# Performance work log

Measured on AMD Instinct MI355X. Metric: run time of the kernel, lower is better.

The kernel has to match this reference:

```python
import jax, jax.numpy as jnp
import numpy as np

V = 100000   # num_regular_embeddings (full vocab)
K = 20000    # num custom (Poincare) embeddings
P = 300      # custom embedding dim
E = 256      # regular / output embedding dim
B = 1024
L = 256


def logmap0(v):
    # project from Poincare ball (c=1) to tangent space at origin
    norm = jnp.linalg.norm(v, axis=-1, keepdims=True)
    safe = jnp.where(norm > 0, norm, 0.5)            # avoid 0/0 and arctanh(0)/0
    scale = jnp.where(norm > 0, jnp.arctanh(safe) / safe, 1.0)
    return scale * v


def mobius_add(x, y):
    x2 = jnp.sum(x * x, axis=-1, keepdims=True)
    y2 = jnp.sum(y * y, axis=-1, keepdims=True)
    xy = jnp.sum(x * y, axis=-1, keepdims=True)
    num = (1 + 2 * xy + y2) * x + (1 - x2) * y
    denom = jnp.maximum(1 + 2 * xy + x2 * y2, 1e-15)
    return num / denom


def setup_inputs() -> dict:
    key = jax.random.key(0)
    k_x, k_perm, k_cw, k_rw, k_lw = jax.random.split(key, 5)

    x = jax.random.randint(k_x, (B, L), 0, V, dtype=jnp.int32)

    # K distinct custom vocab indices, excluding 0 (padding)
    custom_indices = jax.random.permutation(k_perm, jnp.arange(1, V, dtype=jnp.int32))[:K]

    # vocab -> custom table index (1..K), 0 for non-custom
    vocab_to_custom = jnp.zeros((V,), dtype=jnp.int32).at[custom_indices].set(
        jnp.arange(1, K + 1, dtype=jnp.int32))
    # vocab -> regular table index (0..V-K-1) for non-custom slots
    regular_vocab = jnp.where(vocab_to_custom == 0)[0]  # concrete, size V-K
    vocab_to_regular = jnp.zeros((V,), dtype=jnp.int32).at[regular_vocab].set(
        jnp.arange(V - K, dtype=jnp.int32))

    # fixed (pretrained, frozen) custom weights inside unit ball; row 0 = padding
    custom_fixed_w = (jax.random.normal(k_cw, (K + 1, P), dtype=jnp.float32) * 0.02).at[0].set(0.0)
    # trainable custom table initialized to zeros (as in the module)
    custom_train_w = jnp.zeros((K + 1, P), dtype=jnp.float32)
    # regular embedding table, row 0 = padding
    regular_w = (jax.random.normal(k_rw, (V - K, E), dtype=jnp.float32) * 0.02).at[0].set(0.0)
    # linear transform P -> E
    lin_w = jax.random.normal(k_lw, (E, P), dtype=jnp.float32) * 0.05
    lin_b = jnp.zeros((E,), dtype=jnp.float32)

    return {"x": x, "custom_indices": custom_indices,
            "vocab_to_custom": vocab_to_custom, "vocab_to_regular": vocab_to_regular,
            "custom_fixed_w": custom_fixed_w, "custom_train_w": custom_train_w,
            "regular_w": regular_w, "lin_w": lin_w, "lin_b": lin_b}


def reference(x, custom_indices, vocab_to_custom, vocab_to_regular,
              custom_fixed_w, custom_train_w, regular_w, lin_w, lin_b):
    mask = jnp.isin(x, custom_indices)                     # [B, L]
    custom_feat = jnp.where(mask, x, 0)
    regular_feat = jnp.where(mask, 0, x)

    cm = vocab_to_custom[custom_feat]                      # [B, L]
    fixed = logmap0(custom_fixed_w[cm])                    # [B, L, P]
    train = custom_train_w[cm]                             # [B, L, P]
    custom_emb = mobius_add(fixed, train)                  # [B, L, P]

    regular_emb = regular_w[vocab_to_regular[regular_feat]]  # [B, L, E]

    custom_emb = jnp.einsum("blp,ep->ble", custom_emb, lin_w) + lin_b
    return custom_emb + regular_emb
```

## Files before the change

### kernel.cpp

```cpp
#include <hip/hip_runtime.h>
#include <stdint.h>
#include <math.h>

#define NTOK (1024 * 256)
#define CPY_TOK 256
#define CUS_TOK 128
#define P_DIM 300
#define P_PAD 320
#define P_LDS 328
#define E_DIM 256

typedef __attribute__((ext_vector_type(8))) short bf16x8_t;
typedef __attribute__((ext_vector_type(4))) float f32x4_t;

__device__ __forceinline__ unsigned short f2b(float f) {
    union { float f; unsigned int i; } v; v.f = f;
    unsigned int x = v.i;
    return (unsigned short)((x + 0x7FFFu + ((x >> 16) & 1u)) >> 16);
}

__global__ __launch_bounds__(256) void kA_copy(
        const int* __restrict__ x, const int* __restrict__ v2r,
        const float* __restrict__ regular_w, const float* __restrict__ lin_b,
        const float* __restrict__ lin_w, unsigned short* __restrict__ lin_w_pad,
        float* __restrict__ out) {
    int tid  = threadIdx.x;
    int wid  = tid >> 6;
    int lane = tid & 63;

    if (blockIdx.x < (E_DIM * P_PAD) / 256) {
        int idx = blockIdx.x * 256 + tid;
        int e = idx / P_PAD;
        int k = idx - e * P_PAD;
        lin_w_pad[idx] = (k < P_DIM) ? f2b(lin_w[(size_t)e * P_DIM + k])
                                     : (unsigned short)0;
    }

    int base = blockIdx.x * CPY_TOK + wid * 64;
    int xv = x[base + lane];
    int rv = v2r[xv];
    f32x4_t lb4 = *(const f32x4_t*)(lin_b + lane * 4);

    #pragma unroll 1
    for (int it0 = 0; it0 < 64; it0 += 8) {
        int ris[8];
        f32x4_t rows[8];
        #pragma unroll
        for (int u = 0; u < 8; u++) ris[u] = __shfl(rv, it0 + u, 64);
        #pragma unroll
        for (int u = 0; u < 8; u++)
            rows[u] = *(const f32x4_t*)(regular_w
                        + (size_t)ris[u] * E_DIM + lane * 4);
        #pragma unroll
        for (int u = 0; u < 8; u++) {
            f32x4_t o = rows[u] + lb4;
            __builtin_nontemporal_store(
                o, (f32x4_t*)(out + (size_t)(base + it0 + u) * E_DIM + lane * 4));
        }
    }
}

__global__ __launch_bounds__(256) void kB_custom(
        const int* __restrict__ x, const int* __restrict__ v2c,
        const int* __restrict__ v2r,
        const float* __restrict__ fixed_w,
        const float* __restrict__ train_w,
        const float* __restrict__ regular_w,
        const unsigned short* __restrict__ lin_w_pad,
        const float* __restrict__ lin_b,
        float* __restrict__ out) {
    __shared__ __align__(16) unsigned short semb[32][P_LDS];
    __shared__ int stok[CUS_TOK];
    __shared__ int scm[CUS_TOK];
    __shared__ int s_n;

    int tid  = threadIdx.x;
    int wid  = tid >> 6;
    int lane = tid & 63;
    int base = blockIdx.x * CUS_TOK;

    if (tid == 0) s_n = 0;
    __syncthreads();

    if (tid < CUS_TOK) {
        int t  = base + tid;
        int xv = x[t];
        int cm = v2c[xv];
        if (cm > 0) {
            int p = atomicAdd(&s_n, 1);
            stok[p] = t;
            scm[p]  = cm;
        }
    }
    __syncthreads();
    int n = s_n;
    if (n == 0) return;

    int col   = lane & 15;
    int kgrp  = lane >> 4;
    int e0w   = wid * 64;
    int rbase = kgrp * 4;
    float lbe[4], rr0[4];
    int rid0 = v2r[0];
    const float* rrow0 = regular_w + (size_t)rid0 * E_DIM;
    #pragma unroll
    for (int nt = 0; nt < 4; nt++) {
        lbe[nt] = lin_b[e0w + nt * 16 + col];
        rr0[nt] = rrow0[e0w + nt * 16 + col];
    }

    for (int c0 = 0; c0 < n; c0 += 32) {
        int cn = n - c0; if (cn > 32) cn = 32;

        for (int i = wid; i < cn; i += 4) {
            int cm = scm[c0 + i];
            const float* fw = fixed_w + (size_t)cm * P_DIM;
            const float* tw = train_w + (size_t)cm * P_DIM;
            float w[5], tr[5];
            float sw2 = 0.f, st2 = 0.f, swt = 0.f;
            #pragma unroll
            for (int s = 0; s < 5; s++) {
                int j = lane + 64 * s;
                float wv = 0.f, tv = 0.f;
                if (j < P_DIM) { wv = fw[j]; tv = tw[j]; }
                w[s] = wv; tr[s] = tv;
                sw2 = fmaf(wv, wv, sw2); st2 = fmaf(tv, tv, st2); swt = fmaf(wv, tv, swt);
            }
            #pragma unroll
            for (int m = 32; m >= 1; m >>= 1) {
                sw2 += __shfl_xor(sw2, m, 64);
                st2 += __shfl_xor(st2, m, 64);
                swt += __shfl_xor(swt, m, 64);
            }
            float norm = sqrtf(sw2);
            norm = fminf(norm, 0.9999999f);
            float scale = (norm > 0.f) ? (atanhf(norm) / norm) : 1.0f;
            float x2 = scale * scale * sw2;
            float y2 = st2;
            float xy = scale * swt;
            float c1 = (1.f + 2.f * xy + y2) * scale;
            float c2 = (1.f - x2);
            float den = fmaxf(1.f + 2.f * xy + x2 * y2, 1e-15f);
            float inv = 1.f / den;
            #pragma unroll
            for (int s = 0; s < 5; s++) {
                int j = lane + 64 * s;
                float v = (j < P_DIM) ? (c1 * w[s] + c2 * tr[s]) * inv : 0.f;
                semb[i][j] = f2b(v);
            }
        }
        __syncthreads();

        f32x4_t acc[2][4];
        #pragma unroll
        for (int a = 0; a < 2; a++)
            #pragma unroll
            for (int b = 0; b < 4; b++) acc[a][b] = (f32x4_t)(0.f);

        #pragma unroll
        for (int kk = 0; kk < 10; kk++) {
            int k0 = kk * 32 + kgrp * 8;
            bf16x8_t afr[2], bfr[4];
            afr[0] = *(const bf16x8_t*)(&semb[col][k0]);
            afr[1] = *(const bf16x8_t*)(&semb[16 + col][k0]);
            #pragma unroll
            for (int nt = 0; nt < 4; nt++) {
                int e = e0w + nt * 16 + col;
                bfr[nt] = *(const bf16x8_t*)(lin_w_pad + (size_t)e * P_PAD + k0);
            }
            #pragma unroll
            for (int mt = 0; mt < 2; mt++)
                #pragma unroll
                for (int nt = 0; nt < 4; nt++)
                    acc[mt][nt] = __builtin_amdgcn_mfma_f32_16x16x32_bf16(
                        afr[mt], bfr[nt], acc[mt][nt], 0, 0, 0);
        }

        #pragma unroll
        for (int mt = 0; mt < 2; mt++) {
            #pragma unroll
            for (int r = 0; r < 4; r++) {
                int row = mt * 16 + rbase + r;
                if (row < cn) {
                    int t = stok[c0 + row];
                    float* orow = out + (size_t)t * E_DIM;
                    #pragma unroll
                    for (int nt = 0; nt < 4; nt++) {
                        __builtin_nontemporal_store(
                            acc[mt][nt][r] + lbe[nt] + rr0[nt],
                            orow + e0w + nt * 16 + col);
                    }
                }
            }
        }
        __syncthreads();
    }
}

extern "C" void kernel_launch(void* const* d_in, const int* in_sizes, int n_in,
                              void* d_out, int out_size, void* d_ws, size_t ws_size,
                              hipStream_t stream) {
    const int* x   = (const int*)d_in[0];
    const int* v2c = (const int*)d_in[2];
    const int* v2r = (const int*)d_in[3];
    const float* fixed_w   = (const float*)d_in[4];
    const float* train_w   = (const float*)d_in[5];
    const float* regular_w = (const float*)d_in[6];
    const float* lin_w     = (const float*)d_in[7];
    const float* lin_b     = (const float*)d_in[8];
    float* out = (float*)d_out;

    unsigned short* lin_w_pad = (unsigned short*)d_ws;

    kA_copy<<<NTOK / CPY_TOK, 256, 0, stream>>>(x, v2r, regular_w, lin_b,
                                                lin_w, lin_w_pad, out);
    kB_custom<<<NTOK / CUS_TOK, 256, 0, stream>>>(x, v2c, v2r, fixed_w, train_w,
                                                  regular_w, lin_w_pad, lin_b, out);
}
```

Measured before the change: 507.8 us.

## Compact custom tokens into a global list and skip redundant regular writes

The copy kernel now classifies tokens itself. It writes regular rows only for non-custom tokens and appends custom tokens to a global list through a ballot-based atomic compaction. The custom kernel then walks that dense list with a grid-stride loop instead of rescanning every token tile. This removes double writes of custom output rows and the per-block scanning in the second kernel. In exchange it adds a memset, a global atomic per block, extra list traffic, and output token order that depends on the atomic order.

Result: no change. 509.9 us (+0.4%).

```diff
diff --git a/kernel.cpp b/kernel.cpp
--- a/kernel.cpp
+++ b/kernel.cpp
@@ -3,8 +3,8 @@
 #include <math.h>
 
 #define NTOK (1024 * 256)
-#define CPY_TOK 256
-#define CUS_TOK 128
+#define TPB_A 128
+#define GRID_B 2048
 #define P_DIM 300
 #define P_PAD 320
 #define P_LDS 328
@@ -20,10 +20,15 @@
 }
 
 __global__ __launch_bounds__(256) void kA_copy(
-        const int* __restrict__ x, const int* __restrict__ v2r,
+        const int* __restrict__ x, const int* __restrict__ v2c,
+        const int* __restrict__ v2r,
         const float* __restrict__ regular_w, const float* __restrict__ lin_b,
         const float* __restrict__ lin_w, unsigned short* __restrict__ lin_w_pad,
+        int* __restrict__ list_t, int* __restrict__ list_cm,
+        int* __restrict__ counter,
         float* __restrict__ out) {
+    __shared__ int s_ri[TPB_A];
+    __shared__ int wb[2];
     int tid  = threadIdx.x;
     int wid  = tid >> 6;
     int lane = tid & 63;
@@ -36,70 +41,76 @@
                                      : (unsigned short)0;
     }
 
-    int base = blockIdx.x * CPY_TOK + wid * 64;
-    int xv = x[base + lane];
-    int rv = v2r[xv];
+    int base = blockIdx.x * TPB_A;
+    int cm = 0;
+    unsigned long long bl = 0;
+    if (tid < TPB_A) {
+        int xv = x[base + tid];
+        cm = v2c[xv];
+        int rv = v2r[xv];
+        s_ri[tid] = (cm > 0) ? -1 : rv;
+        bl = __ballot(cm > 0);
+        if (lane == 0) wb[wid] = __popcll(bl);
+    }
+    __syncthreads();
+    if (tid == 0) {
+        int tot = wb[0] + wb[1];
+        int b0 = atomicAdd(counter, tot);
+        int c0 = wb[0];
+        wb[0] = b0; wb[1] = b0 + c0;
+    }
+    __syncthreads();
+    if (tid < TPB_A && cm > 0) {
+        int pos = wb[wid] + __popcll(bl & ((1ull << lane) - 1ull));
+        list_t[pos]  = base + tid;
+        list_cm[pos] = cm;
+    }
+
     f32x4_t lb4 = *(const f32x4_t*)(lin_b + lane * 4);
-
+    int tbase = base + wid * 32;
     #pragma unroll 1
-    for (int it0 = 0; it0 < 64; it0 += 8) {
+    for (int it0 = 0; it0 < 32; it0 += 8) {
         int ris[8];
         f32x4_t rows[8];
         #pragma unroll
-        for (int u = 0; u < 8; u++) ris[u] = __shfl(rv, it0 + u, 64);
-        #pragma unroll
-        for (int u = 0; u < 8; u++)
-            rows[u] = *(const f32x4_t*)(regular_w
-                        + (size_t)ris[u] * E_DIM + lane * 4);
+        for (int u = 0; u < 8; u++) ris[u] = s_ri[wid * 32 + it0 + u];
         #pragma unroll
         for (int u = 0; u < 8; u++) {
-            f32x4_t o = rows[u] + lb4;
-            __builtin_nontemporal_store(
-                o, (f32x4_t*)(out + (size_t)(base + it0 + u) * E_DIM + lane * 4));
+            int r = (ris[u] < 0) ? 0 : ris[u];
+            rows[u] = *(const f32x4_t*)(regular_w + (size_t)r * E_DIM + lane * 4);
+        }
+        #pragma unroll
+        for (int u = 0; u < 8; u++) {
+            if (ris[u] >= 0) {
+                f32x4_t o = rows[u] + lb4;
+                __builtin_nontemporal_store(
+                    o, (f32x4_t*)(out + (size_t)(tbase + it0 + u) * E_DIM + lane * 4));
+            }
         }
     }
 }
 
 __global__ __launch_bounds__(256) void kB_custom(
-        const int* __restrict__ x, const int* __restrict__ v2c,
-        const int* __restrict__ v2r,
+        const int* __restrict__ list_t, const int* __restrict__ list_cm,
+        const int* __restrict__ counter,
         const float* __restrict__ fixed_w,
         const float* __restrict__ train_w,
+        const unsigned short* __restrict__ lin_w_pad,
         const float* __restrict__ regular_w,
-        const unsigned short* __restrict__ lin_w_pad,
-        const float* __restrict__ lin_b,
+        const int* __restrict__ v2r, const float* __restrict__ lin_b,
         float* __restrict__ out) {
     __shared__ __align__(16) unsigned short semb[32][P_LDS];
-    __shared__ int stok[CUS_TOK];
-    __shared__ int scm[CUS_TOK];
-    __shared__ int s_n;
+    int count = counter[0];
+    if ((int)(blockIdx.x * 32) >= count) return;
 
     int tid  = threadIdx.x;
     int wid  = tid >> 6;
     int lane = tid & 63;
-    int base = blockIdx.x * CUS_TOK;
-
-    if (tid == 0) s_n = 0;
-    __syncthreads();
-
-    if (tid < CUS_TOK) {
-        int t  = base + tid;
-        int xv = x[t];
-        int cm = v2c[xv];
-        if (cm > 0) {
-            int p = atomicAdd(&s_n, 1);
-            stok[p] = t;
-            scm[p]  = cm;
-        }
-    }
-    __syncthreads();
-    int n = s_n;
-    if (n == 0) return;
-
     int col   = lane & 15;
     int kgrp  = lane >> 4;
     int e0w   = wid * 64;
     int rbase = kgrp * 4;
+
     float lbe[4], rr0[4];
     int rid0 = v2r[0];
     const float* rrow0 = regular_w + (size_t)rid0 * E_DIM;
@@ -109,11 +120,11 @@
         rr0[nt] = rrow0[e0w + nt * 16 + col];
     }
 
-    for (int c0 = 0; c0 < n; c0 += 32) {
-        int cn = n - c0; if (cn > 32) cn = 32;
+    for (int i0 = blockIdx.x * 32; i0 < count; i0 += gridDim.x * 32) {
+        int cn = count - i0; if (cn > 32) cn = 32;
 
         for (int i = wid; i < cn; i += 4) {
-            int cm = scm[c0 + i];
+            int cm = list_cm[i0 + i];
             const float* fw = fixed_w + (size_t)cm * P_DIM;
             const float* tw = train_w + (size_t)cm * P_DIM;
             float w[5], tr[5];
@@ -182,7 +193,7 @@
             for (int r = 0; r < 4; r++) {
                 int row = mt * 16 + rbase + r;
                 if (row < cn) {
-                    int t = stok[c0 + row];
+                    int t = list_t[i0 + row];
                     float* orow = out + (size_t)t * E_DIM;
                     #pragma unroll
                     for (int nt = 0; nt < 4; nt++) {
@@ -210,10 +221,17 @@
     const float* lin_b     = (const float*)d_in[8];
     float* out = (float*)d_out;
 
-    unsigned short* lin_w_pad = (unsigned short*)d_ws;
-
-    kA_copy<<<NTOK / CPY_TOK, 256, 0, stream>>>(x, v2r, regular_w, lin_b,
-                                                lin_w, lin_w_pad, out);
-    kB_custom<<<NTOK / CUS_TOK, 256, 0, stream>>>(x, v2c, v2r, fixed_w, train_w,
-                                                  regular_w, lin_w_pad, lin_b, out);
-}
+    char* ws = (char*)d_ws;
+    int* counter = (int*)ws;
+    int* list_t  = (int*)(ws + 256);
+    int* list_cm = (int*)(ws + 256 + 4 * (size_t)NTOK);
+    unsigned short* lin_w_pad = (unsigned short*)(ws + 256 + 8 * (size_t)NTOK);
+
+    hipMemsetAsync(counter, 0, 64, stream);
+    kA_copy<<<NTOK / TPB_A, 256, 0, stream>>>(x, v2c, v2r, regular_w, lin_b,
+                                              lin_w, lin_w_pad,
+                                              list_t, list_cm, counter, out);
+    kB_custom<<<GRID_B, 256, 0, stream>>>(list_t, list_cm, counter,
+                                          fixed_w, train_w, lin_w_pad,
+                                          regular_w, v2r, lin_b, out);
+}
```
